# Optimization experiments

Measured on AMD Instinct MI355X. Metric: run time of the kernel, lower is better.

The kernel has to match this reference:

```python
import jax, jax.numpy as jnp
import numpy as np
from jax import lax

HUMAN_CONF = 0.7
IOU_TH = 0.5


def setup_inputs() -> dict:
    key = jax.random.key(0)
    k1, k2 = jax.random.split(key)
    B, Q, C = 16, 2048, 2
    return {
        "human_logits": jax.random.normal(k1, (B, Q, C), dtype=jnp.float32),
        "pred_boxes": jax.random.uniform(k2, (B, Q, 4), dtype=jnp.float32),  # cxcywh in [0,1]
        "img_h": 800,
        "img_w": 1333,
    }


def box_cxcywh_to_xyxy(b):
    cx, cy, w, h = b[..., 0], b[..., 1], b[..., 2], b[..., 3]
    return jnp.stack([cx - 0.5 * w, cy - 0.5 * h, cx + 0.5 * w, cy + 0.5 * h], axis=-1)


def pairwise_iou(b):
    # b: [Q,4] xyxy -> iou: [Q,Q]
    area = jnp.clip(b[:, 2] - b[:, 0], 0) * jnp.clip(b[:, 3] - b[:, 1], 0)
    lt = jnp.maximum(b[:, None, :2], b[None, :, :2])
    rb = jnp.minimum(b[:, None, 2:], b[None, :, 2:])
    wh = jnp.clip(rb - lt, 0)
    inter = wh[..., 0] * wh[..., 1]
    union = area[:, None] + area[None, :] - inter
    return inter / jnp.maximum(union, 1e-9)


def nms_keep(boxes, scores, valid, iou_th):
    # Greedy NMS on one image with fixed shapes; returns keep mask [Q].
    Q = scores.shape[0]
    order = jnp.argsort(jnp.where(valid, -scores, jnp.inf))  # valid boxes first, score desc
    b = boxes[order]
    v = valid[order]
    iou = pairwise_iou(b)                       # [Q,Q]
    idx = jnp.arange(Q)
    sup_mat = (iou > iou_th) & (idx[None, :] > idx[:, None])  # i suppresses later j

    def step(supp, i):
        keep_i = v[i] & jnp.logical_not(supp[i])
        supp = supp | (keep_i & sup_mat[i])
        return supp, keep_i

    _, keep_sorted = lax.scan(step, jnp.zeros(Q, bool), idx)
    return jnp.zeros(Q, bool).at[order].set(keep_sorted)


def reference(human_logits, pred_boxes, img_h, img_w):
    prob = jax.nn.softmax(human_logits, axis=-1)          # [B,Q,C]
    scores = prob.max(axis=-1)                            # [B,Q]
    labels = prob.argmax(axis=-1)                         # [B,Q]
    boxes = box_cxcywh_to_xyxy(pred_boxes)                # [B,Q,4]
    scale = jnp.array([img_w, img_h, img_w, img_h], dtype=boxes.dtype)
    boxes = boxes * scale
    valid = (labels == 0) & (scores >= HUMAN_CONF)
    keep = jax.vmap(lambda b, s, v: nms_keep(b, s, v, IOU_TH))(boxes, scores, valid)
    scores_out = jnp.where(keep, scores, 0.0)
    boxes_out = jnp.where(keep[..., None], boxes, 0.0).astype(jnp.int32)
    return scores_out, boxes_out, keep
```

## Files before the change

### kernel.cpp

```cpp
#include <hip/hip_runtime.h>
#include <math.h>


#define QN     2048
#define NS     1024
#define NSLICE 16
#define MATW   17408
#define MAGIC  0x5ca1ab1eu

__device__ __forceinline__ int rb32(int wb) { return 64 * wb * (33 - wb); }

__device__ __forceinline__ unsigned long long shfl_xor_u64(unsigned long long x, int m) {
    int lo = __shfl_xor((int)(unsigned)(x & 0xffffffffull), m, 64);
    int hi = __shfl_xor((int)(unsigned)(x >> 32), m, 64);
    return ((unsigned long long)(unsigned)hi << 32) | (unsigned)lo;
}

__device__ __forceinline__ unsigned long long score_key(float2 l, int q, bool* valid_out) {
    float mx = fmaxf(l.x, l.y), mn = fminf(l.x, l.y);
    float e = expf(mn - mx);
    float score = 1.0f / (1.0f + e);
    bool valid = (l.x >= l.y) && (score >= 0.7f);
    *valid_out = valid;
    unsigned sbits = valid ? __float_as_uint(score) : 0u;
    return ((unsigned long long)(~sbits) << 32) | (unsigned)q;
}

__global__ __launch_bounds__(1024) void kfused(
    const float* __restrict__ logits, const float* __restrict__ pboxes,
    const int* __restrict__ img_h_p, const int* __restrict__ img_w_p,
    unsigned* __restrict__ wflag, unsigned* __restrict__ wmat,
    float* __restrict__ out, int B)
{
    __shared__ __align__(16) char smem[110848];
    unsigned long long* skey = (unsigned long long*)smem;
    float* sx1 = (float*)(smem + 8192);
    float* sy1 = (float*)(smem + 12288);
    float* sx2 = (float*)(smem + 16384);
    float* sy2 = (float*)(smem + 20480);
    float* sar = (float*)(smem + 24576);
    unsigned short* sidxl = (unsigned short*)(smem + 28672);
    int* sMp = (int*)(smem + 32896);
    unsigned long long* skeyB = (unsigned long long*)(smem + 33024);
    unsigned* skm = (unsigned*)(smem + 33024);
    unsigned* smat = (unsigned*)(smem + 41216);

    const int blk = blockIdx.x;
    const int b = blk % B, slice = blk / B;
    const int tid = threadIdx.x, lane = tid & 63, wave = tid >> 6;
    const float sw = (float)(*img_w_p), sh = (float)(*img_h_p);
    const long BQ = (long)B * QN;

    if (tid == 0) *sMp = 0;
    __syncthreads();

    const unsigned long long lmask_lt = (1ull << lane) - 1ull;
#pragma unroll
    for (int qq = 0; qq < 2; ++qq) {
        int q = tid + qq * 1024;
        float2 l = ((const float2*)logits)[b * QN + q];
        bool valid;
        unsigned long long key = score_key(l, q, &valid);
        unsigned long long mb = __ballot(valid);
        int base = 0;
        if (lane == 0 && mb) base = atomicAdd(sMp, __popcll(mb));
        base = __shfl(base, 0, 64);
        if (valid) {
            int slot = base + __popcll(mb & lmask_lt);
            if (slot < NS) skey[slot] = key;
        }
    }
    __syncthreads();
    const int M = *sMp;

    if (M <= NS) {
        unsigned long long v = (tid < M) ? skey[tid] : ~0ull;
        __syncthreads();
#pragma unroll
        for (int k = 2; k <= 64; k <<= 1) {
            bool dir = ((tid & k) == 0);
#pragma unroll
            for (int j = k >> 1; j > 0; j >>= 1) {
                unsigned long long o = shfl_xor_u64(v, j);
                bool takeMin = (dir == ((tid & j) == 0));
                v = ((v < o) == takeMin) ? v : o;
            }
        }
        int pp = 0;
        for (int k = 128; k <= NS; k <<= 1) {
            bool dir = ((tid & k) == 0);
            for (int j = k >> 1; j >= 64; j >>= 1) {
                unsigned long long* buf = pp ? skeyB : skey;
                pp ^= 1;
                buf[tid] = v;
                __syncthreads();
                unsigned long long o = buf[tid ^ j];
                bool takeMin = (dir == ((tid & j) == 0));
                v = ((v < o) == takeMin) ? v : o;
            }
#pragma unroll
            for (int j = 32; j > 0; j >>= 1) {
                unsigned long long o = shfl_xor_u64(v, j);
                bool takeMin = (dir == ((tid & j) == 0));
                v = ((v < o) == takeMin) ? v : o;
            }
        }
        int qi = (int)((unsigned)v & 0xffffu);
        sidxl[tid] = (unsigned short)qi;
        float x1 = 0.f, y1 = 0.f, x2 = 0.f, y2 = 0.f, ar = 0.f;
        if (tid < M) {
            float4 pb = ((const float4*)pboxes)[b * QN + qi];
            x1 = (pb.x - 0.5f * pb.z) * sw;
            y1 = (pb.y - 0.5f * pb.w) * sh;
            x2 = (pb.x + 0.5f * pb.z) * sw;
            y2 = (pb.y + 0.5f * pb.w) * sh;
            ar = fmaxf(x2 - x1, 0.f) * fmaxf(y2 - y1, 0.f);
        }
        sx1[tid] = x1; sy1[tid] = y1; sx2[tid] = x2; sy2[tid] = y2; sar[tid] = ar;
        __syncthreads();

        unsigned* mat = wmat + (long)b * MATW;
        const int NG = (M + 3) >> 2;
        const int W64 = (M + 63) >> 6;
        for (int gi = slice * 16 + wave; gi < NG; gi += 256) {
            const int g = gi << 2;
            const int nr = min(4, M - g);
            const int wb = g >> 6;
            const int rl = 32 - 2 * wb;
            float ax1[4], ay1[4], ax2[4], ay2[4], aar[4];
            int rbase[4];
#pragma unroll
            for (int r = 0; r < 4; ++r) {
                int i = g + min(r, nr - 1);
                ax1[r] = sx1[i]; ay1[r] = sy1[i];
                ax2[r] = sx2[i]; ay2[r] = sy2[i]; aar[r] = sar[i];
                rbase[r] = rb32(wb) + ((g + r) & 63) * rl;
            }
            for (int w = wb; w < W64; ++w) {
                int j = (w << 6) | lane;
                float bx1 = sx1[j], by1 = sy1[j], bx2 = sx2[j], by2 = sy2[j], bar = sar[j];
#pragma unroll
                for (int r = 0; r < 4; ++r) {
                    float ltx = fmaxf(ax1[r], bx1), lty = fmaxf(ay1[r], by1);
                    float rbx = fminf(ax2[r], bx2), rby = fminf(ay2[r], by2);
                    float wx = fmaxf(rbx - ltx, 0.f), wy = fmaxf(rby - lty, 0.f);
                    float inter = wx * wy;
                    float uni = aar[r] + bar - inter;
                    float iou = inter / fmaxf(uni, 1e-9f);
                    bool sup = (iou > 0.5f) && (j > g + r);
                    unsigned long long bal = __ballot(sup);
                    if (lane == 0 && r < nr)
                        *(unsigned long long*)(mat + rbase[r] + 2 * (w - wb)) = bal;
                }
            }
        }
    }

    if (tid < 128) {
        int q = slice * 128 + tid;
        int base = b * QN + q;
        out[base] = 0.f;
        out[BQ * 5 + base] = 0.f;
        float4 z; z.x = 0.f; z.y = 0.f; z.z = 0.f; z.w = 0.f;
        ((float4*)(out + BQ))[base] = z;
    }

    __syncthreads();
    if (tid == 0)
        __hip_atomic_store(&wflag[b * NSLICE + slice], MAGIC,
                           __ATOMIC_RELEASE, __HIP_MEMORY_SCOPE_AGENT);
    if (slice != 0) return;

    if (wave == 0) {
        const unsigned* fp = &wflag[b * NSLICE + (lane & (NSLICE - 1))];
        for (;;) {
            unsigned f = (lane < NSLICE)
                ? __hip_atomic_load(fp, __ATOMIC_ACQUIRE, __HIP_MEMORY_SCOPE_AGENT)
                : MAGIC;
            if (__all(f == MAGIC)) break;
            __builtin_amdgcn_s_sleep(2);
        }
    }
    __syncthreads();

    if (M <= NS) {
        const int W64 = (M + 63) >> 6;
        const int nw4 = rb32(W64) >> 2;
        const uint4* gm4 = (const uint4*)(wmat + (long)b * MATW);
        uint4* sm4 = (uint4*)smat;
        for (int i = tid; i < nw4; i += 1024) sm4[i] = gm4[i];
        __syncthreads();

        if (tid < 64) {
            const unsigned* gm = smat;
            unsigned rem = 0;
            const int Ms = __builtin_amdgcn_readfirstlane(M);
            const int C = (Ms + 31) >> 5;
            const int lam = min(tid, 31);
            unsigned rcur[32];
            for (int c = 0; c < C; ++c) {
                const int wb = c >> 1, rl = 32 - 2 * wb;
                const int half = (c & 1) << 5;
                const int Lc = min(max(tid, 2 * wb), 31);
                const int rb0 = rb32(wb) + half * rl + (Lc - 2 * wb);
#pragma unroll
                for (int t = 0; t < 32; ++t) rcur[t] = gm[rb0 + t * rl];
                unsigned diag = gm[rb32(wb) + (half + lam) * rl + (c - 2 * wb)];

                int lim = min(32, Ms - (c << 5));
                unsigned limmask = (lim >= 32) ? 0xFFFFFFFFu : ((1u << lim) - 1u);
                unsigned rw = ((unsigned)__builtin_amdgcn_readlane((int)rem, c))
                              | ~limmask;
                unsigned keepmask = 0;
#pragma unroll
                for (int t = 0; t < 32; ++t) {
                    unsigned keep = ((~rw) >> t) & 1u;
                    unsigned rword = (unsigned)__builtin_amdgcn_readlane((int)diag, t);
                    rw |= (0u - keep) & rword;
                    keepmask |= keep << t;
                }
#pragma unroll
                for (int t = 0; t < 32; ++t)
                    rem |= (0u - ((keepmask >> t) & 1u)) & rcur[t];
                if (tid == 0) skm[c] = keepmask;
            }
        }
        __syncthreads();

        for (int s = tid; s < M; s += 1024) {
            if ((skm[s >> 5] >> (s & 31)) & 1u) {
                int qi = sidxl[s];
                int base = b * QN + qi;
                float2 l = ((const float2*)logits)[base];
                float e = expf(fminf(l.x, l.y) - fmaxf(l.x, l.y));
                float score = 1.0f / (1.0f + e);
                float4 pb = ((const float4*)pboxes)[base];
                float x1 = (pb.x - 0.5f * pb.z) * sw, y1 = (pb.y - 0.5f * pb.w) * sh;
                float x2 = (pb.x + 0.5f * pb.z) * sw, y2 = (pb.y + 0.5f * pb.w) * sh;
                out[base] = score;
                out[BQ * 5 + base] = 1.f;
                float4 ob;
                ob.x = truncf(x1); ob.y = truncf(y1);
                ob.z = truncf(x2); ob.w = truncf(y2);
                ((float4*)(out + BQ))[base] = ob;
            }
        }
    } else {
        unsigned long long* skeyF = (unsigned long long*)smem;
        unsigned char* ssupp = (unsigned char*)(smem + 16384);
        unsigned char* keepqF = (unsigned char*)(smem + 18432);
        for (int qq = tid; qq < QN; qq += 1024) {
            float2 l = ((const float2*)logits)[b * QN + qq];
            bool valid;
            skeyF[qq] = score_key(l, qq, &valid);
        }
        keepqF[tid] = 0; keepqF[tid + 1024] = 0;
        __syncthreads();
        for (int k = 2; k <= QN; k <<= 1)
            for (int j = k >> 1; j > 0; j >>= 1) {
                int i = ((tid & ~(j - 1)) << 1) | (tid & (j - 1));
                int p = i | j;
                bool up = ((i & k) == 0);
                unsigned long long a = skeyF[i], c2 = skeyF[p];
                if ((a > c2) == up) { skeyF[i] = c2; skeyF[p] = a; }
                __syncthreads();
            }
        for (int s = tid; s < M; s += 1024) ssupp[s] = 0;
        __syncthreads();
        for (int i = 0; i < M; ++i) {
            __syncthreads();
            if (ssupp[i]) continue;
            int ia = (unsigned short)(unsigned)skeyF[i];
            float4 pa = ((const float4*)pboxes)[b * QN + ia];
            float ax1 = (pa.x - 0.5f * pa.z) * sw, ay1 = (pa.y - 0.5f * pa.w) * sh;
            float ax2 = (pa.x + 0.5f * pa.z) * sw, ay2 = (pa.y + 0.5f * pa.w) * sh;
            float areaA = fmaxf(ax2 - ax1, 0.f) * fmaxf(ay2 - ay1, 0.f);
            for (int jj = i + 1 + tid; jj < M; jj += 1024) {
                int jb = (unsigned short)(unsigned)skeyF[jj];
                float4 pq = ((const float4*)pboxes)[b * QN + jb];
                float bx1 = (pq.x - 0.5f * pq.z) * sw, by1 = (pq.y - 0.5f * pq.w) * sh;
                float bx2 = (pq.x + 0.5f * pq.z) * sw, by2 = (pq.y + 0.5f * pq.w) * sh;
                float ltx = fmaxf(ax1, bx1), lty = fmaxf(ay1, by1);
                float rbx = fminf(ax2, bx2), rby = fminf(ay2, by2);
                float wx = fmaxf(rbx - ltx, 0.f), wy = fmaxf(rby - lty, 0.f);
                float inter = wx * wy;
                float areaB = fmaxf(bx2 - bx1, 0.f) * fmaxf(by2 - by1, 0.f);
                float uni = areaA + areaB - inter;
                if (inter / fmaxf(uni, 1e-9f) > 0.5f) ssupp[jj] = 1;
            }
        }
        __syncthreads();
        for (int s = tid; s < M; s += 1024)
            if (!ssupp[s]) keepqF[(unsigned short)(unsigned)skeyF[s]] = 1;
        __syncthreads();
#pragma unroll
        for (int qq = 0; qq < 2; ++qq) {
            int q = tid + qq * 1024;
            int base = b * QN + q;
            float2 l = ((const float2*)logits)[base];
            float e = expf(fminf(l.x, l.y) - fmaxf(l.x, l.y));
            float score = 1.0f / (1.0f + e);
            float4 pb = ((const float4*)pboxes)[base];
            float x1 = (pb.x - 0.5f * pb.z) * sw, y1 = (pb.y - 0.5f * pb.w) * sh;
            float x2 = (pb.x + 0.5f * pb.z) * sw, y2 = (pb.y + 0.5f * pb.w) * sh;
            int kp = keepqF[q];
            out[base] = kp ? score : 0.f;
            out[BQ * 5 + base] = kp ? 1.f : 0.f;
            float4 ob;
            ob.x = kp ? truncf(x1) : 0.f;
            ob.y = kp ? truncf(y1) : 0.f;
            ob.z = kp ? truncf(x2) : 0.f;
            ob.w = kp ? truncf(y2) : 0.f;
            ((float4*)(out + BQ))[base] = ob;
        }
    }
}

extern "C" void kernel_launch(void* const* d_in, const int* in_sizes, int n_in,
                              void* d_out, int out_size, void* d_ws, size_t ws_size,
                              hipStream_t stream) {
    const float* logits = (const float*)d_in[0];
    const float* pboxes = (const float*)d_in[1];
    const int*   img_h  = (const int*)d_in[2];
    const int*   img_w  = (const int*)d_in[3];
    float* out = (float*)d_out;
    const int B = in_sizes[0] / (QN * 2);

    char* ws = (char*)d_ws;
    unsigned* wflag = (unsigned*)(ws + 0);
    unsigned* wmat  = (unsigned*)(ws + 1024);

    kfused<<<dim3(B * NSLICE), dim3(1024), 0, stream>>>(logits, pboxes, img_h, img_w,
                                                        wflag, wmat, out, B);
}
```

Measured before the change: 97.13 us.

## Double-buffer NMS scan row loads and split row OR across wave halves

The serial greedy scan now prefetches the next 32-column chunk's suppression rows and diagonal word into a second register buffer while it processes the current chunk. Each half of the 64-lane wave handles 16 of the 32 rows, and the two halves combine their results with a cross-half shuffle, which halves the per-lane loads and ORs. The matrix-build loop also changes how row groups are assigned to waves and slices. This is meant to hide LDS load latency on the single-wave critical path, at the cost of one extra shuffle per chunk and more complex control flow.

Result: no change. 95.47 us (-1.7%).

```diff
diff --git a/kernel.cpp b/kernel.cpp
--- a/kernel.cpp
+++ b/kernel.cpp
@@ -25,6 +25,38 @@
     unsigned sbits = valid ? __float_as_uint(score) : 0u;
     return ((unsigned long long)(~sbits) << 32) | (unsigned)q;
 }
+
+#define SCAN_LOAD(RBUF, DIAG, c) do {                                         \
+    const int wb_ = (c) >> 1, rl_ = 32 - 2 * wb_;                             \
+    const int half_ = ((c) & 1) << 5;                                         \
+    const int Lc_ = min(max((int)(tid & 31), 2 * wb_), 31);                   \
+    const int rb0_ = rb32(wb_) + half_ * rl_ + (Lc_ - 2 * wb_);               \
+    _Pragma("unroll")                                                         \
+    for (int t = 0; t < 16; ++t) RBUF[t] = gm[rb0_ + (tb + t) * rl_];         \
+    DIAG = gm[rb32(wb_) + (half_ + lam) * rl_ + ((c) - 2 * wb_)];             \
+} while (0)
+
+#define SCAN_PROC(RBUF, DIAG, c) do {                                         \
+    int lim_ = min(32, Ms - ((c) << 5));                                      \
+    unsigned limmask_ = (lim_ >= 32) ? 0xFFFFFFFFu : ((1u << lim_) - 1u);     \
+    unsigned rw_ = ((unsigned)__builtin_amdgcn_readlane((int)rem, (c)))       \
+                   | ~limmask_;                                               \
+    unsigned keepmask_ = 0;                                                   \
+    _Pragma("unroll")                                                         \
+    for (int t = 0; t < 32; ++t) {                                            \
+        unsigned keep_ = ((~rw_) >> t) & 1u;                                  \
+        unsigned rword_ = (unsigned)__builtin_amdgcn_readlane((int)(DIAG), t);\
+        rw_ |= (0u - keep_) & rword_;                                         \
+        keepmask_ |= keep_ << t;                                              \
+    }                                                                         \
+    unsigned part_ = 0;                                                       \
+    _Pragma("unroll")                                                         \
+    for (int t = 0; t < 16; ++t)                                              \
+        part_ |= (0u - ((keepmask_ >> (tb + t)) & 1u)) & RBUF[t];             \
+    part_ |= (unsigned)__shfl_xor((int)part_, 32, 64);                        \
+    rem |= part_;                                                             \
+    if (tid == 0) skm[(c)] = keepmask_;                                       \
+} while (0)
 
 __global__ __launch_bounds__(1024) void kfused(
     const float* __restrict__ logits, const float* __restrict__ pboxes,
@@ -122,7 +154,7 @@
         unsigned* mat = wmat + (long)b * MATW;
         const int NG = (M + 3) >> 2;
         const int W64 = (M + 63) >> 6;
-        for (int gi = slice * 16 + wave; gi < NG; gi += 256) {
+        for (int gi = slice + 16 * wave; gi < NG; gi += 256) {
             const int g = gi << 2;
             const int nr = min(4, M - g);
             const int wb = g >> 6;
@@ -197,32 +229,16 @@
             const int Ms = __builtin_amdgcn_readfirstlane(M);
             const int C = (Ms + 31) >> 5;
             const int lam = min(tid, 31);
-            unsigned rcur[32];
-            for (int c = 0; c < C; ++c) {
-                const int wb = c >> 1, rl = 32 - 2 * wb;
-                const int half = (c & 1) << 5;
-                const int Lc = min(max(tid, 2 * wb), 31);
-                const int rb0 = rb32(wb) + half * rl + (Lc - 2 * wb);
-#pragma unroll
-                for (int t = 0; t < 32; ++t) rcur[t] = gm[rb0 + t * rl];
-                unsigned diag = gm[rb32(wb) + (half + lam) * rl + (c - 2 * wb)];
-
-                int lim = min(32, Ms - (c << 5));
-                unsigned limmask = (lim >= 32) ? 0xFFFFFFFFu : ((1u << lim) - 1u);
-                unsigned rw = ((unsigned)__builtin_amdgcn_readlane((int)rem, c))
-                              | ~limmask;
-                unsigned keepmask = 0;
-#pragma unroll
-                for (int t = 0; t < 32; ++t) {
-                    unsigned keep = ((~rw) >> t) & 1u;
-                    unsigned rword = (unsigned)__builtin_amdgcn_readlane((int)diag, t);
-                    rw |= (0u - keep) & rword;
-                    keepmask |= keep << t;
+            const int tb = (tid >> 5) << 4;
+            unsigned rA[16], rB[16], diagA = 0, diagB = 0;
+            if (C > 0) SCAN_LOAD(rA, diagA, 0);
+            for (int c = 0; c < C; c += 2) {
+                if (c + 1 < C) SCAN_LOAD(rB, diagB, c + 1);
+                SCAN_PROC(rA, diagA, c);
+                if (c + 1 < C) {
+                    if (c + 2 < C) SCAN_LOAD(rA, diagA, c + 2);
+                    SCAN_PROC(rB, diagB, c + 1);
                 }
-#pragma unroll
-                for (int t = 0; t < 32; ++t)
-                    rem |= (0u - ((keepmask >> t) & 1u)) & rcur[t];
-                if (tid == 0) skm[c] = keepmask;
             }
         }
         __syncthreads();
```
